# Optimization experiments

Measured on AMD Instinct MI355X. Metric: run time of the kernel, lower is better.

Reference implementation:

```python
import jax, jax.numpy as jnp
import numpy as np
from functools import partial

B, D, E, O, K = 65536, 64, 16, 512, 2  # batch, feat dim, num_experts, output_size, top-k


def setup_inputs() -> dict:
    key = jax.random.key(0)
    k1, k2, k3, k4, k5 = jax.random.split(key, 5)
    scale_g = 1.0 / np.sqrt(D)
    return {
        "x": jax.random.normal(k1, (B, D), dtype=jnp.float32),
        "wg": jax.random.uniform(k2, (D, E), dtype=jnp.float32, minval=-scale_g, maxval=scale_g),
        "bg": jnp.zeros((E,), dtype=jnp.float32),
        "We": jax.random.uniform(k3, (E, D, O), dtype=jnp.float32, minval=-scale_g, maxval=scale_g),
        "be": jax.random.uniform(k4, (E, O), dtype=jnp.float32, minval=-scale_g, maxval=scale_g),
    }


def reference(x, wg, bg, We, be):
    # --- gating (noisy_gating=False / eval path) ---
    logits = jax.nn.softmax(x @ wg + bg, axis=1)            # [B, E]
    top_vals, top_idx = jax.lax.top_k(logits, K)            # [B, K]
    top_gates = top_vals / (jnp.sum(top_vals, axis=1, keepdims=True) + 1e-6)
    rows = jnp.arange(x.shape[0])[:, None]                  # [B, 1]
    gates = jnp.zeros_like(logits).at[rows, top_idx].set(top_gates)  # dense [B, E], sparse rows

    # --- dispatch / per-expert linear / gated scatter-combine ---
    # Equivalent dense-masked form of SparseDispatcher: y[i] = sum_e gates[i,e] * (x[i] @ We[e] + be[e])
    def step(y, ewb):
        w, b, g = ewb                                       # [D,O], [O], [B]
        return y + g[:, None] * (x @ w + b), None

    y0 = jnp.zeros((x.shape[0], We.shape[2]), dtype=x.dtype)
    y, _ = jax.lax.scan(step, y0, (We, be, gates.T))
    return y
```

## Files before the change

### kernel.cpp

```cpp
#include <hip/hip_runtime.h>

typedef unsigned int u32;
typedef unsigned short u16;
typedef float f4 __attribute__((ext_vector_type(4)));
typedef __bf16 b8 __attribute__((ext_vector_type(8)));
typedef unsigned short us8 __attribute__((ext_vector_type(8)));

#define DD 64
#define NE 16
#define OO 512
#define TR 64

struct __align__(16) Tile { u32 pid, slot, nr, pad; };

union U8 { us8 u; b8 b; };

__device__ __forceinline__ u16 f2bf(float f) {
  u32 u = __float_as_uint(f);
  u32 r = (u + 0x7fffu + ((u >> 16) & 1u)) >> 16;
  return (u16)r;
}

__global__ void k_wt(const float* __restrict__ We, u16* __restrict__ WeT) {
  __shared__ float tl[64][65];
  int b = blockIdx.x;
  int e = b >> 3;
  int oc = (b & 7) * 64;
  int t = threadIdx.x;
  int d = t >> 2, seg = (t & 3) * 16;
  const f4* src = (const f4*)(We + ((size_t)(e * DD + d)) * OO + oc + seg);
  f4 v0 = src[0], v1 = src[1], v2 = src[2], v3 = src[3];
#pragma unroll
  for (int j = 0; j < 4; j++) {
    tl[d][seg + j]      = v0[j];
    tl[d][seg + 4 + j]  = v1[j];
    tl[d][seg + 8 + j]  = v2[j];
    tl[d][seg + 12 + j] = v3[j];
  }
  __syncthreads();
  int o = t >> 2, ds = (t & 3) * 16;
  us8 o0, o1;
#pragma unroll
  for (int j = 0; j < 8; j++) {
    o0[j] = f2bf(tl[ds + j][o]);
    o1[j] = f2bf(tl[ds + 8 + j][o]);
  }
  u16* dst = WeT + ((size_t)(e * OO + oc + o)) * DD + ds;
  *(us8*)dst = o0;
  *(us8*)(dst + 8) = o1;
}

__global__ void k_gate(const float* __restrict__ x, const float* __restrict__ wg,
                       const float* __restrict__ bg, u32* __restrict__ hist,
                       u32* __restrict__ pid_arr, float* __restrict__ glo_arr,
                       float* __restrict__ ghi_arr) {
  __shared__ u32 hcnt[256];
  int t = threadIdx.x;
  hcnt[t] = 0;
  __syncthreads();
  int row = blockIdx.x * 256 + t;

  float l[NE];
#pragma unroll
  for (int e = 0; e < NE; e++) l[e] = bg[e];

  const f4* xp = (const f4*)(x + (size_t)row * DD);
  for (int d4 = 0; d4 < 16; d4++) {
    f4 xv = xp[d4];
#pragma unroll
    for (int qq = 0; qq < 4; qq++) {
      float xs = xv[qq];
      const float* wrow = wg + (d4 * 4 + qq) * NE;
#pragma unroll
      for (int e = 0; e < NE; e++) l[e] = fmaf(xs, wrow[e], l[e]);
    }
  }
  float mx = l[0];
#pragma unroll
  for (int e = 1; e < NE; e++) mx = fmaxf(mx, l[e]);
  float Z = 0.f;
#pragma unroll
  for (int e = 0; e < NE; e++) Z += __expf(l[e] - mx);
  int i1 = 0; float b1 = l[0];
#pragma unroll
  for (int e = 1; e < NE; e++) { if (l[e] > b1) { b1 = l[e]; i1 = e; } }
  int i2 = -1; float b2 = -1e30f;
#pragma unroll
  for (int e = 0; e < NE; e++) { if (e != i1 && l[e] > b2) { b2 = l[e]; i2 = e; } }
  float p1 = __expf(b1 - mx) / Z;
  float p2 = __expf(b2 - mx) / Z;
  float den = p1 + p2 + 1e-6f;
  float g1 = p1 / den, g2 = p2 / den;
  int elo, ehi; float glo, ghi;
  if (i1 < i2) { elo = i1; ehi = i2; glo = g1; ghi = g2; }
  else         { elo = i2; ehi = i1; glo = g2; ghi = g1; }
  u32 pid = (u32)(elo * NE + ehi);
  pid_arr[row] = pid;
  glo_arr[row] = glo;
  ghi_arr[row] = ghi;
  atomicAdd(&hcnt[pid], 1u);
  __syncthreads();
  hist[blockIdx.x * 256 + t] = hcnt[t];
}

__global__ void k_colscan(u32* __restrict__ hist, u32* __restrict__ tot) {
  __shared__ u32 s[256];
  int b = threadIdx.x, p = blockIdx.x;
  u32 v = hist[b * 256 + p];
  s[b] = v;
  __syncthreads();
  for (int d = 1; d < 256; d <<= 1) {
    u32 a = 0;
    if (b >= d) a = s[b - d];
    __syncthreads();
    s[b] += a;
    __syncthreads();
  }
  hist[b * 256 + p] = s[b] - v;
  if (b == 255) tot[p] = s[255];
}

__global__ void k_base(const u32* __restrict__ tot, u32* __restrict__ base,
                       u32* __restrict__ ntp, Tile* __restrict__ tiles) {
  __shared__ u32 s[256], s2[256];
  int t = threadIdx.x;
  u32 v = tot[t];
  u32 nt = (v + (TR - 1)) >> 6;
  s[t] = v; s2[t] = nt;
  __syncthreads();
  for (int d = 1; d < 256; d <<= 1) {
    u32 a = 0, c = 0;
    if (t >= d) { a = s[t - d]; c = s2[t - d]; }
    __syncthreads();
    s[t] += a; s2[t] += c;
    __syncthreads();
  }
  u32 rb = s[t] - v;
  u32 tb = s2[t] - nt;
  base[t] = rb;
  for (u32 k = 0; k < nt; k++) {
    Tile td;
    td.pid = (u32)t;
    td.slot = rb + k * (u32)TR;
    u32 rem = v - k * (u32)TR;
    td.nr = rem < (u32)TR ? rem : (u32)TR;
    td.pad = 0;
    tiles[tb + k] = td;
  }
  if (t == 255) *ntp = s2[255];
}

__global__ void k_scatter(const u32* __restrict__ pid_arr, const u32* __restrict__ hist,
                          const u32* __restrict__ base, u32* __restrict__ sorted) {
  __shared__ u32 lcnt[256], lbase[256];
  int t = threadIdx.x;
  lcnt[t] = 0;
  lbase[t] = base[t];
  __syncthreads();
  int row = blockIdx.x * 256 + t;
  u32 pid = pid_arr[row];
  u32 rank = atomicAdd(&lcnt[pid], 1u);
  u32 off = lbase[pid] + hist[blockIdx.x * 256 + pid];
  sorted[off + rank] = (u32)row;
}

__global__ __launch_bounds__(256, 3)
void k_moe(const float* __restrict__ x, const u16* __restrict__ WeT,
           const float* __restrict__ be, const u32* __restrict__ sorted,
           const u32* __restrict__ ntp, const Tile* __restrict__ tiles,
           const float* __restrict__ glo_arr, const float* __restrict__ ghi_arr,
           float* __restrict__ y) {
  __shared__ __align__(16) u16 Xl[TR * 72];
  __shared__ u32 rid_s[TR];
  __shared__ float glo_s[TR], ghi_s[TR];

  u32 bid = blockIdx.x;
  if (bid >= *ntp) return;
  Tile td = tiles[bid];
  u32 e_lo = td.pid >> 4, e_hi = td.pid & 15u;
  u32 slot0 = td.slot, nr = td.nr;

  int t = threadIdx.x;
  if (t < TR) {
    u32 i = (u32)t;
    u32 slot = slot0 + ((i < nr) ? i : 0u);
    u32 r = sorted[slot];
    rid_s[t] = r;
    bool valid = i < nr;
    glo_s[t] = valid ? glo_arr[r] : 0.f;
    ghi_s[t] = valid ? ghi_arr[r] : 0.f;
  }
  __syncthreads();
  {
    int i = t >> 2;
    int seg = (t & 3) * 16;
    u32 r = rid_s[i];
    const f4* xp = (const f4*)(x + (size_t)r * DD + seg);
    f4 v0 = xp[0], v1 = xp[1], v2 = xp[2], v3 = xp[3];
    float vv[16] = { v0[0], v0[1], v0[2], v0[3], v1[0], v1[1], v1[2], v1[3],
                     v2[0], v2[1], v2[2], v2[3], v3[0], v3[1], v3[2], v3[3] };
    us8 o0, o1;
#pragma unroll
    for (int j = 0; j < 8; j++) { o0[j] = f2bf(vv[j]); o1[j] = f2bf(vv[8 + j]); }
    *(us8*)&Xl[i * 72 + seg] = o0;
    *(us8*)&Xl[i * 72 + seg + 8] = o1;
  }
  __syncthreads();

  int lane = t & 63;
  int w = t >> 6;
  int q = lane >> 4;
  int ln = lane & 15;

  b8 xfr[4][2];
#pragma unroll
  for (int rt = 0; rt < 4; rt++)
#pragma unroll
    for (int kc = 0; kc < 2; kc++) {
      U8 tmp; tmp.u = *(const us8*)&Xl[(rt * 16 + ln) * 72 + kc * 32 + q * 8];
      xfr[rt][kc] = tmp.b;
    }

  float gl[4], gh[4];
  bool vld[4];
  float* yp[4];
#pragma unroll
  for (int rt = 0; rt < 4; rt++) {
    int i = rt * 16 + ln;
    gl[rt] = glo_s[i];
    gh[rt] = ghi_s[i];
    vld[rt] = (u32)i < nr;
    yp[rt] = y + (size_t)rid_s[i] * OO;
  }

  const u16* wlo = WeT + (size_t)e_lo * OO * DD;
  const u16* whi = WeT + (size_t)e_hi * OO * DD;
  const f4 zero = {0.f, 0.f, 0.f, 0.f};

#pragma unroll 2
  for (int ct = 0; ct < 8; ct++) {
    int colA = w * 128 + ct * 16 + ln;
    int colq = w * 128 + ct * 16 + q * 4;
    const us8* plo = (const us8*)(wlo + (size_t)colA * DD + q * 8);
    const us8* phi = (const us8*)(whi + (size_t)colA * DD + q * 8);
    U8 t0, t1, t2, t3;
    t0.u = plo[0]; t1.u = plo[4];
    t2.u = phi[0]; t3.u = phi[4];
    b8 wl0 = t0.b, wl1 = t1.b, wh0 = t2.b, wh1 = t3.b;
    f4 bl = *(const f4*)(be + e_lo * OO + colq);
    f4 bh = *(const f4*)(be + e_hi * OO + colq);

#pragma unroll
    for (int rt = 0; rt < 4; rt++) {
      f4 aL = zero, aH = zero;
      aL = __builtin_amdgcn_mfma_f32_16x16x32_bf16(wl0, xfr[rt][0], aL, 0, 0, 0);
      aL = __builtin_amdgcn_mfma_f32_16x16x32_bf16(wl1, xfr[rt][1], aL, 0, 0, 0);
      aH = __builtin_amdgcn_mfma_f32_16x16x32_bf16(wh0, xfr[rt][0], aH, 0, 0, 0);
      aH = __builtin_amdgcn_mfma_f32_16x16x32_bf16(wh1, xfr[rt][1], aH, 0, 0, 0);
      if (vld[rt]) {
        f4 v;
#pragma unroll
        for (int r = 0; r < 4; r++)
          v[r] = gl[rt] * (aL[r] + bl[r]) + gh[rt] * (aH[r] + bh[r]);
        *(f4*)(yp[rt] + colq) = v;
      }
    }
  }
}

extern "C" void kernel_launch(void* const* d_in, const int* in_sizes, int n_in,
                              void* d_out, int out_size, void* d_ws, size_t ws_size,
                              hipStream_t stream) {
  const float* x  = (const float*)d_in[0];
  const float* wg = (const float*)d_in[1];
  const float* bg = (const float*)d_in[2];
  const float* We = (const float*)d_in[3];
  const float* be = (const float*)d_in[4];
  float* y = (float*)d_out;

  char* ws = (char*)d_ws;
  u32* ntp     = (u32*)(ws + 0);
  Tile* tiles  = (Tile*)(ws + 4096);
  u32* pid_arr = (u32*)(ws + 32768);
  float* glo_a = (float*)(ws + 32768 + 262144);
  float* ghi_a = (float*)(ws + 32768 + 2 * 262144);
  u32* sorted  = (u32*)(ws + 32768 + 3 * 262144);
  u16* WeT     = (u16*)(ws + 32768 + 4 * 262144);
  u32* hist    = (u32*)(ws + 32768 + 4 * 262144 + 1048576);
  u32* tot     = (u32*)(ws + 32768 + 4 * 262144 + 1048576 + 262144);
  u32* base    = (u32*)(ws + 32768 + 4 * 262144 + 1048576 + 262144 + 1024);

  k_wt<<<128, 256, 0, stream>>>(We, WeT);
  k_gate<<<256, 256, 0, stream>>>(x, wg, bg, hist, pid_arr, glo_a, ghi_a);
  k_colscan<<<256, 256, 0, stream>>>(hist, tot);
  k_base<<<1, 256, 0, stream>>>(tot, base, ntp, tiles);
  k_scatter<<<256, 256, 0, stream>>>(pid_arr, hist, base, sorted);
  k_moe<<<1144, 256, 0, stream>>>(x, WeT, be, sorted, ntp, tiles, glo_a, ghi_a, y);
}
```

Measured before the change: 199.7 us.

## Merge preprocessing kernels and replace column scan with single-block transposed scan

Fuses the weight transpose and gating kernels into one launch that branches on block index, and replaces the column-scan and base kernels with a single 1024-thread block. That block scans a transposed histogram in shared-memory chunks and then builds the tile list. This cuts the launch count from six to four and removes one round of global histogram traffic. The cost is a serial single-block step, which may take longer than the parallel 256-block scan it replaces.

Result: slower. 207.1 us (+3.7%).

```diff
diff --git a/kernel.cpp b/kernel.cpp
--- a/kernel.cpp
+++ b/kernel.cpp
@@ -5,6 +5,7 @@
 typedef float f4 __attribute__((ext_vector_type(4)));
 typedef __bf16 b8 __attribute__((ext_vector_type(8)));
 typedef unsigned short us8 __attribute__((ext_vector_type(8)));
+typedef unsigned int u4 __attribute__((ext_vector_type(4)));
 
 #define DD 64
 #define NE 16
@@ -21,44 +22,47 @@
   return (u16)r;
 }
 
-__global__ void k_wt(const float* __restrict__ We, u16* __restrict__ WeT) {
+__global__ void k_front(const float* __restrict__ We, u16* __restrict__ WeT,
+                        const float* __restrict__ x, const float* __restrict__ wg,
+                        const float* __restrict__ bg, u32* __restrict__ hist_t,
+                        u32* __restrict__ pid_arr, float* __restrict__ glo_arr,
+                        float* __restrict__ ghi_arr) {
   __shared__ float tl[64][65];
-  int b = blockIdx.x;
-  int e = b >> 3;
-  int oc = (b & 7) * 64;
-  int t = threadIdx.x;
-  int d = t >> 2, seg = (t & 3) * 16;
-  const f4* src = (const f4*)(We + ((size_t)(e * DD + d)) * OO + oc + seg);
-  f4 v0 = src[0], v1 = src[1], v2 = src[2], v3 = src[3];
-#pragma unroll
-  for (int j = 0; j < 4; j++) {
-    tl[d][seg + j]      = v0[j];
-    tl[d][seg + 4 + j]  = v1[j];
-    tl[d][seg + 8 + j]  = v2[j];
-    tl[d][seg + 12 + j] = v3[j];
-  }
-  __syncthreads();
-  int o = t >> 2, ds = (t & 3) * 16;
-  us8 o0, o1;
-#pragma unroll
-  for (int j = 0; j < 8; j++) {
-    o0[j] = f2bf(tl[ds + j][o]);
-    o1[j] = f2bf(tl[ds + 8 + j][o]);
-  }
-  u16* dst = WeT + ((size_t)(e * OO + oc + o)) * DD + ds;
-  *(us8*)dst = o0;
-  *(us8*)(dst + 8) = o1;
-}
-
-__global__ void k_gate(const float* __restrict__ x, const float* __restrict__ wg,
-                       const float* __restrict__ bg, u32* __restrict__ hist,
-                       u32* __restrict__ pid_arr, float* __restrict__ glo_arr,
-                       float* __restrict__ ghi_arr) {
   __shared__ u32 hcnt[256];
   int t = threadIdx.x;
+
+  if (blockIdx.x < 128) {
+    int b = blockIdx.x;
+    int e = b >> 3;
+    int oc = (b & 7) * 64;
+    int d = t >> 2, seg = (t & 3) * 16;
+    const f4* src = (const f4*)(We + ((size_t)(e * DD + d)) * OO + oc + seg);
+    f4 v0 = src[0], v1 = src[1], v2 = src[2], v3 = src[3];
+#pragma unroll
+    for (int j = 0; j < 4; j++) {
+      tl[d][seg + j]      = v0[j];
+      tl[d][seg + 4 + j]  = v1[j];
+      tl[d][seg + 8 + j]  = v2[j];
+      tl[d][seg + 12 + j] = v3[j];
+    }
+    __syncthreads();
+    int o = t >> 2, ds = (t & 3) * 16;
+    us8 o0, o1;
+#pragma unroll
+    for (int j = 0; j < 8; j++) {
+      o0[j] = f2bf(tl[ds + j][o]);
+      o1[j] = f2bf(tl[ds + 8 + j][o]);
+    }
+    u16* dst = WeT + ((size_t)(e * OO + oc + o)) * DD + ds;
+    *(us8*)dst = o0;
+    *(us8*)(dst + 8) = o1;
+    return;
+  }
+
+  int gb = blockIdx.x - 128;
   hcnt[t] = 0;
   __syncthreads();
-  int row = blockIdx.x * 256 + t;
+  int row = gb * 256 + t;
 
   float l[NE];
 #pragma unroll
@@ -100,57 +104,76 @@
   ghi_arr[row] = ghi;
   atomicAdd(&hcnt[pid], 1u);
   __syncthreads();
-  hist[blockIdx.x * 256 + t] = hcnt[t];
-}
-
-__global__ void k_colscan(u32* __restrict__ hist, u32* __restrict__ tot) {
-  __shared__ u32 s[256];
-  int b = threadIdx.x, p = blockIdx.x;
-  u32 v = hist[b * 256 + p];
-  s[b] = v;
+  hist_t[t * 256 + gb] = hcnt[t];
+}
+
+__global__ __launch_bounds__(1024)
+void k_mid(u32* __restrict__ hist_t, u32* __restrict__ base,
+           u32* __restrict__ ntp, Tile* __restrict__ tiles) {
+  __shared__ __align__(16) u32 ch[64 * 256];
+  __shared__ u32 tot_s[256], s[256], s2[256];
+  int t = threadIdx.x;
+
+  for (int c = 0; c < 4; c++) {
+#pragma unroll
+    for (int i = 0; i < 4; i++)
+      ((u4*)ch)[t + i * 1024] = ((const u4*)(hist_t + c * 16384))[t + i * 1024];
+    __syncthreads();
+    int pc = t >> 4, k = t & 15;
+    u32* row = ch + pc * 256;
+    u32 vals[16]; u32 sum = 0;
+#pragma unroll
+    for (int j = 0; j < 16; j++) { vals[j] = row[k * 16 + j]; sum += vals[j]; }
+    u32 pre = sum;
+#pragma unroll
+    for (int d = 1; d < 16; d <<= 1) {
+      u32 up = __shfl_up(pre, d, 16);
+      if (k >= d) pre += up;
+    }
+    u32 run = pre - sum;
+#pragma unroll
+    for (int j = 0; j < 16; j++) { u32 v = vals[j]; row[k * 16 + j] = run; run += v; }
+    if (k == 15) tot_s[c * 64 + pc] = run;
+    __syncthreads();
+#pragma unroll
+    for (int i = 0; i < 4; i++)
+      ((u4*)(hist_t + c * 16384))[t + i * 1024] = ((u4*)ch)[t + i * 1024];
+    __syncthreads();
+  }
+
+  if (t < 256) {
+    u32 v = tot_s[t];
+    u32 nt = (v + (TR - 1)) >> 6;
+    s[t] = v; s2[t] = nt;
+  }
   __syncthreads();
   for (int d = 1; d < 256; d <<= 1) {
-    u32 a = 0;
-    if (b >= d) a = s[b - d];
-    __syncthreads();
-    s[b] += a;
-    __syncthreads();
-  }
-  hist[b * 256 + p] = s[b] - v;
-  if (b == 255) tot[p] = s[255];
-}
-
-__global__ void k_base(const u32* __restrict__ tot, u32* __restrict__ base,
-                       u32* __restrict__ ntp, Tile* __restrict__ tiles) {
-  __shared__ u32 s[256], s2[256];
-  int t = threadIdx.x;
-  u32 v = tot[t];
-  u32 nt = (v + (TR - 1)) >> 6;
-  s[t] = v; s2[t] = nt;
-  __syncthreads();
-  for (int d = 1; d < 256; d <<= 1) {
-    u32 a = 0, c = 0;
-    if (t >= d) { a = s[t - d]; c = s2[t - d]; }
-    __syncthreads();
-    s[t] += a; s2[t] += c;
-    __syncthreads();
-  }
-  u32 rb = s[t] - v;
-  u32 tb = s2[t] - nt;
-  base[t] = rb;
-  for (u32 k = 0; k < nt; k++) {
-    Tile td;
-    td.pid = (u32)t;
-    td.slot = rb + k * (u32)TR;
-    u32 rem = v - k * (u32)TR;
-    td.nr = rem < (u32)TR ? rem : (u32)TR;
-    td.pad = 0;
-    tiles[tb + k] = td;
-  }
-  if (t == 255) *ntp = s2[255];
-}
-
-__global__ void k_scatter(const u32* __restrict__ pid_arr, const u32* __restrict__ hist,
+    u32 a = 0, c2 = 0;
+    if (t < 256 && t >= d) { a = s[t - d]; c2 = s2[t - d]; }
+    __syncthreads();
+    if (t < 256) { s[t] += a; s2[t] += c2; }
+    __syncthreads();
+  }
+  if (t < 256) {
+    u32 v = tot_s[t];
+    u32 nt = (v + (TR - 1)) >> 6;
+    u32 rb = s[t] - v;
+    u32 tb = s2[t] - nt;
+    base[t] = rb;
+    for (u32 kk = 0; kk < nt; kk++) {
+      Tile td;
+      td.pid = (u32)t;
+      td.slot = rb + kk * (u32)TR;
+      u32 rem = v - kk * (u32)TR;
+      td.nr = rem < (u32)TR ? rem : (u32)TR;
+      td.pad = 0;
+      tiles[tb + kk] = td;
+    }
+    if (t == 255) *ntp = s2[255];
+  }
+}
+
+__global__ void k_scatter(const u32* __restrict__ pid_arr, const u32* __restrict__ hist_t,
                           const u32* __restrict__ base, u32* __restrict__ sorted) {
   __shared__ u32 lcnt[256], lbase[256];
   int t = threadIdx.x;
@@ -160,7 +183,7 @@
   int row = blockIdx.x * 256 + t;
   u32 pid = pid_arr[row];
   u32 rank = atomicAdd(&lcnt[pid], 1u);
-  u32 off = lbase[pid] + hist[blockIdx.x * 256 + pid];
+  u32 off = lbase[pid] + hist_t[pid * 256 + blockIdx.x];
   sorted[off + rank] = (u32)row;
 }
 
@@ -286,14 +309,11 @@
   float* ghi_a = (float*)(ws + 32768 + 2 * 262144);
   u32* sorted  = (u32*)(ws + 32768 + 3 * 262144);
   u16* WeT     = (u16*)(ws + 32768 + 4 * 262144);
-  u32* hist    = (u32*)(ws + 32768 + 4 * 262144 + 1048576);
-  u32* tot     = (u32*)(ws + 32768 + 4 * 262144 + 1048576 + 262144);
-  u32* base    = (u32*)(ws + 32768 + 4 * 262144 + 1048576 + 262144 + 1024);
-
-  k_wt<<<128, 256, 0, stream>>>(We, WeT);
-  k_gate<<<256, 256, 0, stream>>>(x, wg, bg, hist, pid_arr, glo_a, ghi_a);
-  k_colscan<<<256, 256, 0, stream>>>(hist, tot);
-  k_base<<<1, 256, 0, stream>>>(tot, base, ntp, tiles);
-  k_scatter<<<256, 256, 0, stream>>>(pid_arr, hist, base, sorted);
+  u32* hist_t  = (u32*)(ws + 32768 + 4 * 262144 + 1048576);
+  u32* base    = (u32*)(ws + 32768 + 4 * 262144 + 1048576 + 262144);
+
+  k_front<<<384, 256, 0, stream>>>(We, WeT, x, wg, bg, hist_t, pid_arr, glo_a, ghi_a);
+  k_mid<<<1, 1024, 0, stream>>>(hist_t, base, ntp, tiles);
+  k_scatter<<<256, 256, 0, stream>>>(pid_arr, hist_t, base, sorted);
   k_moe<<<1144, 256, 0, stream>>>(x, WeT, be, sorted, ntp, tiles, glo_a, ghi_a, y);
 }
```
